# Performance work log

Measured on AMD Instinct MI355X. Metric: run time of the kernel, lower is better.

The kernel has to match this reference:

```python
import jax, jax.numpy as jnp
import numpy as np

H = 8      # n_heads
DK = 64    # d_k per head
EPS = 1e-5       # InstanceNorm1d eps
SLOPE = 0.01     # LeakyReLU negative slope


def setup_inputs() -> dict:
    key = jax.random.key(0)
    ks = jax.random.split(key, 6)
    B, C, L = 16, 256, 1024
    HD = H * DK  # 512
    return {
        "x": jax.random.normal(ks[0], (B, C, L), dtype=jnp.float32),
        "Wq": jax.random.normal(ks[1], (HD, C), dtype=jnp.float32) * 0.02,
        "Wk": jax.random.normal(ks[2], (HD, C), dtype=jnp.float32) * 0.02,
        "Wv": jax.random.normal(ks[3], (HD, C), dtype=jnp.float32) * 0.02,
        "Wo": jax.random.normal(ks[4], (C, HD), dtype=jnp.float32) * 0.02,
        "gamma": jax.random.normal(ks[5], (1,), dtype=jnp.float32),
    }


def reference(x, Wq, Wk, Wv, Wo, gamma):
    B, C, L = x.shape
    # conv1x1 projections (bias=False) == channel matmuls -> [B, H*DK, L]
    # then reshape/permute into heads: [B, H, L, DK]
    def proj(W):
        y = jnp.einsum('oc,bcl->bol', W, x)          # [B, H*DK, L]
        return y.reshape(B, H, DK, L).transpose(0, 1, 3, 2)  # [B, H, L, DK]

    q, k, v = proj(Wq), proj(Wk), proj(Wv)
    # softmax-free linear attention: (Q K^T / d_k) V
    logits = jnp.einsum('bhld,bhmd->bhlm', q, k) / DK  # [B, H, L, L]
    out = jnp.einsum('bhlm,bhmd->bhld', logits, v)     # [B, H, L, DK]
    # merge heads back to channel-first [B, H*DK, L]
    merged = out.transpose(0, 1, 3, 2).reshape(B, H * DK, L)
    # output conv1x1 -> [B, C, L]
    o = jnp.einsum('oc,bcl->bol', Wo, merged)
    # InstanceNorm1d (affine=False): normalize over L per (b, c)
    mu = jnp.mean(o, axis=-1, keepdims=True)
    var = jnp.var(o, axis=-1, keepdims=True)
    o = (o - mu) * jax.lax.rsqrt(var + EPS)
    # gamma-scaled residual + LeakyReLU
    y = o * gamma + x
    return jnp.where(y >= 0, y, SLOPE * y)
```

## Files before the change

### kernel.cpp

```cpp
#include <hip/hip_runtime.h>

typedef __bf16 bf16;
typedef bf16 bf16x8 __attribute__((ext_vector_type(8)));
typedef bf16 bf16x4 __attribute__((ext_vector_type(4)));
typedef float f32x4 __attribute__((ext_vector_type(4)));

#define EPS 1e-5f
#define SLOPE 0.01f

__device__ __forceinline__ void gld_lds16(const bf16* g, bf16* l) {
    __builtin_amdgcn_global_load_lds(
        (const __attribute__((address_space(1))) unsigned int*)g,
        (__attribute__((address_space(3))) unsigned int*)l, 16, 0, 0);
}

__global__ __launch_bounds__(256) void prep_kernel(
    const float* __restrict__ x,
    const float* __restrict__ Wq, const float* __restrict__ Wk,
    const float* __restrict__ Wv, const float* __restrict__ Wo,
    bf16* __restrict__ xT, bf16* __restrict__ xB,
    bf16* __restrict__ WkB, bf16* __restrict__ WvB,
    bf16* __restrict__ WoB, bf16* __restrict__ WqT)
{
    __shared__ float tile[64][65];
    const int id = blockIdx.x;
    const int t = threadIdx.x;
    if (id < 1024) {
        const int lt = id & 15, ct = (id >> 4) & 3, b = id >> 6;
        {
            const int cl = t >> 2;
            const int l4 = (t & 3) << 4;
            const float* src = x + (size_t)(b * 256 + ct * 64 + cl) * 1024 + lt * 64 + l4;
            float4 v0 = ((const float4*)src)[0];
            float4 v1 = ((const float4*)src)[1];
            float4 v2 = ((const float4*)src)[2];
            float4 v3 = ((const float4*)src)[3];
            bf16x8 r0, r1;
            r0[0]=(bf16)v0.x; r0[1]=(bf16)v0.y; r0[2]=(bf16)v0.z; r0[3]=(bf16)v0.w;
            r0[4]=(bf16)v1.x; r0[5]=(bf16)v1.y; r0[6]=(bf16)v1.z; r0[7]=(bf16)v1.w;
            r1[0]=(bf16)v2.x; r1[1]=(bf16)v2.y; r1[2]=(bf16)v2.z; r1[3]=(bf16)v2.w;
            r1[4]=(bf16)v3.x; r1[5]=(bf16)v3.y; r1[6]=(bf16)v3.z; r1[7]=(bf16)v3.w;
            bf16* xbd = xB + (size_t)(b * 256 + ct * 64 + cl) * 1024 + lt * 64 + l4;
            *(bf16x8*)xbd = r0;
            *(bf16x8*)(xbd + 8) = r1;
            float* tr = &tile[cl][l4];
            tr[0]=v0.x; tr[1]=v0.y; tr[2]=v0.z; tr[3]=v0.w;
            tr[4]=v1.x; tr[5]=v1.y; tr[6]=v1.z; tr[7]=v1.w;
            tr[8]=v2.x; tr[9]=v2.y; tr[10]=v2.z; tr[11]=v2.w;
            tr[12]=v3.x; tr[13]=v3.y; tr[14]=v3.z; tr[15]=v3.w;
        }
        __syncthreads();
        {
            const int lw = t >> 2;
            const int ec = (t & 3) << 4;
            bf16x8 o0, o1;
            #pragma unroll
            for (int ii = 0; ii < 8; ++ii) {
                o0[ii] = (bf16)tile[ec + ii][lw];
                o1[ii] = (bf16)tile[ec + 8 + ii][lw];
            }
            bf16* dst = xT + (size_t)(b * 1024 + lt * 64 + lw) * 256 + ct * 64 + ec;
            *(bf16x8*)dst = o0;
            *(bf16x8*)(dst + 8) = o1;
        }
    } else if (id < 1408) {
        const int i = (id - 1024) * 1024 + t * 4;
        const float* src; bf16* dst;
        if (i < 131072)      { src = Wk + i;            dst = WkB + i; }
        else if (i < 262144) { src = Wv + (i - 131072); dst = WvB + (i - 131072); }
        else                 { src = Wo + (i - 262144); dst = WoB + (i - 262144); }
        float4 v = *(const float4*)src;
        bf16x4 o;
        o[0]=(bf16)v.x; o[1]=(bf16)v.y; o[2]=(bf16)v.z; o[3]=(bf16)v.w;
        *(bf16x4*)dst = o;
    } else {
        const int id2 = id - 1408;
        const int h = id2 >> 2, ct = id2 & 3;
        {
            const int e  = t >> 2;
            const int c4 = (t & 3) << 4;
            const float* src = Wq + (size_t)(h * 64 + e) * 256 + ct * 64 + c4;
            float4 v0 = ((const float4*)src)[0];
            float4 v1 = ((const float4*)src)[1];
            float4 v2 = ((const float4*)src)[2];
            float4 v3 = ((const float4*)src)[3];
            float* tr = &tile[e][c4];
            tr[0]=v0.x; tr[1]=v0.y; tr[2]=v0.z; tr[3]=v0.w;
            tr[4]=v1.x; tr[5]=v1.y; tr[6]=v1.z; tr[7]=v1.w;
            tr[8]=v2.x; tr[9]=v2.y; tr[10]=v2.z; tr[11]=v2.w;
            tr[12]=v3.x; tr[13]=v3.y; tr[14]=v3.z; tr[15]=v3.w;
        }
        __syncthreads();
        {
            const int c  = t >> 2;
            const int e4 = (t & 3) << 4;
            bf16x8 o0, o1;
            #pragma unroll
            for (int ii = 0; ii < 8; ++ii) {
                o0[ii] = (bf16)tile[e4 + ii][c];
                o1[ii] = (bf16)tile[e4 + 8 + ii][c];
            }
            bf16* dst = WqT + (size_t)h * 16384 + (size_t)(ct * 64 + c) * 64 + e4;
            *(bf16x8*)dst = o0;
            *(bf16x8*)(dst + 8) = o1;
        }
    }
}

template<int KDIM, typename OutT>
__global__ __launch_bounds__(256) void gemm128_bt(
    const bf16* __restrict__ A, const bf16* __restrict__ Bt, OutT* __restrict__ C,
    long long sA, long long sBt, long long sC, int ldC)
{
    constexpr int NT = KDIM / 32;
    constexpr int NB = 5;
    __shared__ bf16 As[NB][128 * 32];
    __shared__ bf16 Bs[NB][128 * 32];
    const int z = blockIdx.z;
    A  += (size_t)z * sA;
    Bt += (size_t)z * sBt;
    C  += (size_t)z * sC;
    const int m0 = blockIdx.x * 128;
    const int n0 = blockIdx.y * 128;
    const int t = threadIdx.x, w = t >> 6, l = t & 63;
    const int srow = w * 16 + (l >> 2);
    const int ske  = (l & 3) * 8;
    const bf16* ga = A  + (size_t)(m0 + srow) * KDIM + ske;
    const bf16* gb = Bt + (size_t)(n0 + srow) * KDIM + ske;
    const int loff = srow * 32 + ske;
    const int lm = l & 15, lq = l >> 4;
    const int wm = (w & 1) * 64, wn = (w >> 1) * 64;

    #pragma unroll
    for (int i = 0; i < NB - 1; ++i) {
        const int k0 = i * 32;
        gld_lds16(ga + k0, &As[i][0] + loff);
        gld_lds16(ga + k0 + (size_t)64 * KDIM, &As[i][0] + 64 * 32 + loff);
        gld_lds16(gb + k0, &Bs[i][0] + loff);
        gld_lds16(gb + k0 + (size_t)64 * KDIM, &Bs[i][0] + 64 * 32 + loff);
    }

    f32x4 acc[4][4] = {};
    #pragma unroll
    for (int kt = 0; kt < NT; ++kt) {
        const int cur = kt % NB;
        const int stg = (kt + NB - 1) % NB;
        const int remain = NT - 1 - kt;
        if (remain >= 3)      asm volatile("s_waitcnt vmcnt(12)" ::: "memory");
        else if (remain == 2) asm volatile("s_waitcnt vmcnt(8)"  ::: "memory");
        else if (remain == 1) asm volatile("s_waitcnt vmcnt(4)"  ::: "memory");
        else                  asm volatile("s_waitcnt vmcnt(0)"  ::: "memory");
        __builtin_amdgcn_s_barrier();
        __builtin_amdgcn_sched_barrier(0);
        if (kt + NB - 1 < NT) {
            const int k0 = (kt + NB - 1) * 32;
            gld_lds16(ga + k0, &As[stg][0] + loff);
            gld_lds16(ga + k0 + (size_t)64 * KDIM, &As[stg][0] + 64 * 32 + loff);
            gld_lds16(gb + k0, &Bs[stg][0] + loff);
            gld_lds16(gb + k0 + (size_t)64 * KDIM, &Bs[stg][0] + 64 * 32 + loff);
        }
        bf16x8 af[4], bfr[4];
        #pragma unroll
        for (int i = 0; i < 4; ++i)
            af[i] = *(const bf16x8*)(&As[cur][0] + (wm + i * 16 + lm) * 32 + lq * 8);
        #pragma unroll
        for (int j = 0; j < 4; ++j)
            bfr[j] = *(const bf16x8*)(&Bs[cur][0] + (wn + j * 16 + lm) * 32 + lq * 8);
        #pragma unroll
        for (int i = 0; i < 4; ++i)
            #pragma unroll
            for (int j = 0; j < 4; ++j)
                acc[i][j] = __builtin_amdgcn_mfma_f32_16x16x32_bf16(af[i], bfr[j], acc[i][j], 0, 0, 0);
    }
    #pragma unroll
    for (int i = 0; i < 4; ++i)
        #pragma unroll
        for (int j = 0; j < 4; ++j) {
            const int row = m0 + wm + i * 16 + lq * 4;
            const int col = n0 + wn + j * 16 + lm;
            OutT* cp = C + (size_t)row * ldC + col;
            #pragma unroll
            for (int r = 0; r < 4; ++r)
                cp[(size_t)r * ldC] = (OutT)acc[i][j][r];
        }
}

template<int KDIM, typename OutT>
__global__ __launch_bounds__(256) void gemm64_bt(
    const bf16* __restrict__ A, const bf16* __restrict__ Bt, OutT* __restrict__ C,
    long long sA, long long sBt, long long sC, int ldC)
{
    constexpr int NT = KDIM / 32;
    constexpr int NB = 5;
    __shared__ bf16 As[NB][64 * 32];
    __shared__ bf16 Bs[NB][64 * 32];
    const int z = blockIdx.z;
    A  += (size_t)z * sA;
    Bt += (size_t)z * sBt;
    C  += (size_t)z * sC;
    const int m0 = blockIdx.x * 64;
    const int n0 = blockIdx.y * 64;
    const int t = threadIdx.x, w = t >> 6, l = t & 63;
    const int srow = t >> 2;
    const int ske  = (t & 3) * 8;
    const bf16* ga = A  + (size_t)(m0 + srow) * KDIM + ske;
    const bf16* gb = Bt + (size_t)(n0 + srow) * KDIM + ske;
    const int loff = srow * 32 + ske;
    const int lm = l & 15, lq = l >> 4;

    #pragma unroll
    for (int i = 0; i < NB - 1; ++i) {
        const int k0 = i * 32;
        gld_lds16(ga + k0, &As[i][0] + loff);
        gld_lds16(gb + k0, &Bs[i][0] + loff);
    }

    f32x4 acc[4] = {};
    #pragma unroll
    for (int kt = 0; kt < NT; ++kt) {
        const int cur = kt % NB;
        const int stg = (kt + NB - 1) % NB;
        const int remain = NT - 1 - kt;
        if (remain >= 3)      asm volatile("s_waitcnt vmcnt(6)" ::: "memory");
        else if (remain == 2) asm volatile("s_waitcnt vmcnt(4)" ::: "memory");
        else if (remain == 1) asm volatile("s_waitcnt vmcnt(2)" ::: "memory");
        else                  asm volatile("s_waitcnt vmcnt(0)" ::: "memory");
        __builtin_amdgcn_s_barrier();
        __builtin_amdgcn_sched_barrier(0);
        if (kt + NB - 1 < NT) {
            const int k0 = (kt + NB - 1) * 32;
            gld_lds16(ga + k0, &As[stg][0] + loff);
            gld_lds16(gb + k0, &Bs[stg][0] + loff);
        }
        bf16x8 af = *(const bf16x8*)(&As[cur][0] + (w * 16 + lm) * 32 + lq * 8);
        bf16x8 bfr[4];
        #pragma unroll
        for (int j = 0; j < 4; ++j)
            bfr[j] = *(const bf16x8*)(&Bs[cur][0] + (j * 16 + lm) * 32 + lq * 8);
        #pragma unroll
        for (int j = 0; j < 4; ++j)
            acc[j] = __builtin_amdgcn_mfma_f32_16x16x32_bf16(af, bfr[j], acc[j], 0, 0, 0);
    }
    #pragma unroll
    for (int j = 0; j < 4; ++j) {
        const int row = m0 + w * 16 + lq * 4;
        const int col = n0 + j * 16 + lm;
        OutT* cp = C + (size_t)row * ldC + col;
        #pragma unroll
        for (int r = 0; r < 4; ++r)
            cp[(size_t)r * ldC] = (OutT)acc[j][r];
    }
}

__global__ __launch_bounds__(256) void tm_kernel(
    const bf16* __restrict__ S, const bf16* __restrict__ WkB,
    const bf16* __restrict__ WqT, bf16* __restrict__ WmT)
{
    __shared__ __align__(16) bf16 Sc[2][8192];
    __shared__ __align__(16) bf16 Kc[2][8192];
    __shared__ __align__(16) bf16 Qb[16384];
    __shared__ __align__(16) bf16 Tb[4096];

    const int bh = blockIdx.x;
    const int b = bh >> 3, h = bh & 7;
    const bf16* Sg = S   + (size_t)b * 131072 + (size_t)h * 64 * 256;
    const bf16* Kg = WkB + (size_t)h * 64 * 256;
    const bf16* Qg = WqT + (size_t)h * 16384;
    const int t = threadIdx.x, w = t >> 6, l = t & 63;
    const int lm = l & 15, lq = l >> 4;

    #pragma unroll
    for (int it = 0; it < 4; ++it) {
        const int idx = it * 256 + t;
        const int r = idx >> 4, s2 = idx & 15;
        const int gs = (s2 ^ (r & 7)) * 8;
        gld_lds16(Sg + (size_t)r * 256 + gs, &Sc[0][0] + r * 128 + s2 * 8);
        gld_lds16(Kg + (size_t)r * 256 + gs, &Kc[0][0] + r * 128 + s2 * 8);
    }
    #pragma unroll
    for (int it = 0; it < 8; ++it) {
        const int idx = it * 256 + t;
        const int r = idx >> 3, s2 = idx & 7;
        gld_lds16(Qg + (size_t)r * 64 + (s2 ^ (r & 7)) * 8, Qb + r * 64 + s2 * 8);
    }
    #pragma unroll
    for (int it = 0; it < 4; ++it) {
        const int idx = it * 256 + t;
        const int r = idx >> 4, s2 = idx & 15;
        const int gs = (s2 ^ (r & 7)) * 8;
        gld_lds16(Sg + (size_t)r * 256 + 128 + gs, &Sc[1][0] + r * 128 + s2 * 8);
        gld_lds16(Kg + (size_t)r * 256 + 128 + gs, &Kc[1][0] + r * 128 + s2 * 8);
    }

    f32x4 accT[4] = {};
    asm volatile("s_waitcnt vmcnt(16)" ::: "memory");
    __builtin_amdgcn_s_barrier();
    __builtin_amdgcn_sched_barrier(0);
    #pragma unroll
    for (int ks = 0; ks < 4; ++ks) {
        const int q = ks * 4 + lq;
        const int ra = w * 16 + lm;
        bf16x8 a = *(const bf16x8*)(&Sc[0][0] + ra * 128 + (q ^ (ra & 7)) * 8);
        #pragma unroll
        for (int nf = 0; nf < 4; ++nf) {
            const int rb = nf * 16 + lm;
            bf16x8 bb = *(const bf16x8*)(&Kc[0][0] + rb * 128 + (q ^ (rb & 7)) * 8);
            accT[nf] = __builtin_amdgcn_mfma_f32_16x16x32_bf16(a, bb, accT[nf], 0, 0, 0);
        }
    }
    asm volatile("s_waitcnt vmcnt(0)" ::: "memory");
    __builtin_amdgcn_s_barrier();
    __builtin_amdgcn_sched_barrier(0);
    #pragma unroll
    for (int ks = 0; ks < 4; ++ks) {
        const int q = ks * 4 + lq;
        const int ra = w * 16 + lm;
        bf16x8 a = *(const bf16x8*)(&Sc[1][0] + ra * 128 + (q ^ (ra & 7)) * 8);
        #pragma unroll
        for (int nf = 0; nf < 4; ++nf) {
            const int rb = nf * 16 + lm;
            bf16x8 bb = *(const bf16x8*)(&Kc[1][0] + rb * 128 + (q ^ (rb & 7)) * 8);
            accT[nf] = __builtin_amdgcn_mfma_f32_16x16x32_bf16(a, bb, accT[nf], 0, 0, 0);
        }
    }
    #pragma unroll
    for (int nf = 0; nf < 4; ++nf)
        #pragma unroll
        for (int ri = 0; ri < 4; ++ri) {
            const int row = w * 16 + lq * 4 + ri;
            const int col = nf * 16 + lm;
            Tb[row * 64 + (((col >> 3) ^ (row & 7)) << 3) + (col & 7)] =
                (bf16)(accT[nf][ri] * 0.015625f);
        }
    __syncthreads();

    f32x4 accM[4][4] = {};
    #pragma unroll
    for (int ks = 0; ks < 2; ++ks) {
        const int q = ks * 4 + lq;
        bf16x8 bfrag[4];
        #pragma unroll
        for (int nf = 0; nf < 4; ++nf) {
            const int rb = nf * 16 + lm;
            bfrag[nf] = *(const bf16x8*)(Tb + rb * 64 + (q ^ (rb & 7)) * 8);
        }
        #pragma unroll
        for (int mf = 0; mf < 4; ++mf) {
            const int ra = w * 64 + mf * 16 + lm;
            bf16x8 a = *(const bf16x8*)(Qb + ra * 64 + (q ^ (ra & 7)) * 8);
            #pragma unroll
            for (int nf = 0; nf < 4; ++nf)
                accM[mf][nf] = __builtin_amdgcn_mfma_f32_16x16x32_bf16(a, bfrag[nf], accM[mf][nf], 0, 0, 0);
        }
    }
    bf16* Wg = WmT + (size_t)b * 131072 + h * 64;
    #pragma unroll
    for (int mf = 0; mf < 4; ++mf)
        #pragma unroll
        for (int nf = 0; nf < 4; ++nf)
            #pragma unroll
            for (int ri = 0; ri < 4; ++ri) {
                const int c = w * 64 + mf * 16 + lq * 4 + ri;
                const int d = nf * 16 + lm;
                Wg[(size_t)c * 512 + d] = (bf16)accM[mf][nf][ri];
            }
}

__global__ __launch_bounds__(256) void norm_kernel(
    const bf16* __restrict__ o, const bf16* __restrict__ xB,
    const float* __restrict__ gamma, float* __restrict__ y)
{
    const size_t row = blockIdx.x;
    const bf16* orow = o + row * 1024;
    const bf16* xrow = xB + row * 1024;
    float* yrow = y + row * 1024;
    const int tid = threadIdx.x;

    bf16x4 ov = *(const bf16x4*)(orow + tid * 4);
    float4 v = {(float)ov[0], (float)ov[1], (float)ov[2], (float)ov[3]};
    float s  = v.x + v.y + v.z + v.w;
    float ss = v.x * v.x + v.y * v.y + v.z * v.z + v.w * v.w;
    #pragma unroll
    for (int off = 32; off > 0; off >>= 1) {
        s  += __shfl_down(s, off);
        ss += __shfl_down(ss, off);
    }
    __shared__ float red[10];
    const int wave = tid >> 6, lane = tid & 63;
    if (lane == 0) { red[wave] = s; red[4 + wave] = ss; }
    __syncthreads();
    if (tid == 0) {
        float a  = red[0] + red[1] + red[2] + red[3];
        float b2 = red[4] + red[5] + red[6] + red[7];
        float mu = a * (1.0f / 1024.0f);
        float var = b2 * (1.0f / 1024.0f) - mu * mu;
        red[8] = mu;
        red[9] = rsqrtf(var + EPS);
    }
    __syncthreads();
    const float mu = red[8], inv = red[9], g = gamma[0];
    bf16x4 xv4 = *(const bf16x4*)(xrow + tid * 4);
    float4 r;
    r.x = (v.x - mu) * inv * g + (float)xv4[0];
    r.y = (v.y - mu) * inv * g + (float)xv4[1];
    r.z = (v.z - mu) * inv * g + (float)xv4[2];
    r.w = (v.w - mu) * inv * g + (float)xv4[3];
    r.x = r.x >= 0.f ? r.x : SLOPE * r.x;
    r.y = r.y >= 0.f ? r.y : SLOPE * r.y;
    r.z = r.z >= 0.f ? r.z : SLOPE * r.z;
    r.w = r.w >= 0.f ? r.w : SLOPE * r.w;
    ((float4*)yrow)[tid] = r;
}

extern "C" void kernel_launch(void* const* d_in, const int* in_sizes, int n_in,
                              void* d_out, int out_size, void* d_ws, size_t ws_size,
                              hipStream_t stream) {
    const float* x     = (const float*)d_in[0];
    const float* Wq    = (const float*)d_in[1];
    const float* Wk    = (const float*)d_in[2];
    const float* Wv    = (const float*)d_in[3];
    const float* Wo    = (const float*)d_in[4];
    const float* gamma = (const float*)d_in[5];
    float* y = (float*)d_out;

    char* wsb = (char*)d_ws;
    bf16* xT  = (bf16*)(wsb);
    bf16* xB  = (bf16*)(wsb +  8388608);
    bf16* WkB = (bf16*)(wsb + 16777216);
    bf16* WvB = (bf16*)(wsb + 17039360);
    bf16* WoB = (bf16*)(wsb + 17301504);
    bf16* WqT = (bf16*)(wsb + 17563648);
    bf16* G   = (bf16*)(wsb + 17825792);
    bf16* S   = (bf16*)(wsb + 19922944);
    bf16* WmT = (bf16*)(wsb + 24117248);
    bf16* Wt  = (bf16*)(wsb + 28311552);
    bf16* o   = (bf16*)(wsb + 30408704);

    prep_kernel<<<dim3(1440), 256, 0, stream>>>(x, Wq, Wk, Wv, Wo, xT, xB, WkB, WvB, WoB, WqT);

    gemm64_bt<1024, bf16><<<dim3(4, 4, 16), 256, 0, stream>>>(
        xB, xB, G, 262144LL, 262144LL, 65536LL, 256);

    gemm64_bt<256, bf16><<<dim3(8, 4, 16), 256, 0, stream>>>(
        WvB, G, S, 0LL, 65536LL, 131072LL, 256);

    tm_kernel<<<dim3(128), 256, 0, stream>>>(S, WkB, WqT, WmT);

    gemm64_bt<512, bf16><<<dim3(4, 4, 16), 256, 0, stream>>>(
        WoB, WmT, Wt, 0LL, 131072LL, 65536LL, 256);

    gemm128_bt<256, bf16><<<dim3(2, 8, 16), 256, 0, stream>>>(
        Wt, xT, o, 65536LL, 262144LL, 262144LL, 1024);

    norm_kernel<<<dim3(4096), 256, 0, stream>>>(o, xB, gamma, y);
}
```

Baseline: 123.8 us.

## Fuse five GEMM/tm launches into one cooperative persistent kernel with grid syncs

Replaces the five separate launches (Gram GEMM, V projection, per-head tm, Wo GEMM, final output GEMM) with one cooperative kernel of 256 blocks. Stages are separated by grid-wide barriers, and shared memory is held in a union sized for the largest stage. The aim is to remove per-launch overhead and tail gaps between the small dependent kernels. The cost is grid.sync latency, occupancy limited by the largest LDS footprint, and idle blocks during the tm stage, which only uses 128 blocks.

```diff
diff --git a/kernel.cpp b/kernel.cpp
--- a/kernel.cpp
+++ b/kernel.cpp
@@ -1,4 +1,7 @@
 #include <hip/hip_runtime.h>
+#include <hip/hip_cooperative_groups.h>
+
+namespace cg = cooperative_groups;
 
 typedef __bf16 bf16;
 typedef bf16 bf16x8 __attribute__((ext_vector_type(8)));
@@ -107,22 +110,80 @@
     }
 }
 
-template<int KDIM, typename OutT>
-__global__ __launch_bounds__(256) void gemm128_bt(
-    const bf16* __restrict__ A, const bf16* __restrict__ Bt, OutT* __restrict__ C,
-    long long sA, long long sBt, long long sC, int ldC)
+struct __align__(16) SmG64  { bf16 As[5][64 * 32];  bf16 Bs[5][64 * 32];  };
+struct __align__(16) SmG128 { bf16 As[5][128 * 32]; bf16 Bs[5][128 * 32]; };
+struct __align__(16) SmTm   { bf16 Sc[2][8192]; bf16 Kc[2][8192];
+                              bf16 Qb[16384];  bf16 Tb[4096]; };
+union __align__(16) SmAll { SmG64 g64; SmG128 g128; SmTm tm; };
+
+template<int KDIM>
+__device__ __forceinline__ void gemm64_body(SmG64& s,
+    const bf16* __restrict__ A, const bf16* __restrict__ Bt, bf16* __restrict__ C,
+    int m0, int n0, int ldC, int t)
 {
     constexpr int NT = KDIM / 32;
     constexpr int NB = 5;
-    __shared__ bf16 As[NB][128 * 32];
-    __shared__ bf16 Bs[NB][128 * 32];
-    const int z = blockIdx.z;
-    A  += (size_t)z * sA;
-    Bt += (size_t)z * sBt;
-    C  += (size_t)z * sC;
-    const int m0 = blockIdx.x * 128;
-    const int n0 = blockIdx.y * 128;
-    const int t = threadIdx.x, w = t >> 6, l = t & 63;
+    const int w = t >> 6, l = t & 63;
+    const int srow = t >> 2;
+    const int ske  = (t & 3) * 8;
+    const bf16* ga = A  + (size_t)(m0 + srow) * KDIM + ske;
+    const bf16* gb = Bt + (size_t)(n0 + srow) * KDIM + ske;
+    const int loff = srow * 32 + ske;
+    const int lm = l & 15, lq = l >> 4;
+
+    __syncthreads();
+
+    #pragma unroll
+    for (int i = 0; i < NB - 1; ++i) {
+        const int k0 = i * 32;
+        gld_lds16(ga + k0, &s.As[i][0] + loff);
+        gld_lds16(gb + k0, &s.Bs[i][0] + loff);
+    }
+    f32x4 acc[4] = {};
+    #pragma unroll
+    for (int kt = 0; kt < NT; ++kt) {
+        const int cur = kt % NB;
+        const int stg = (kt + NB - 1) % NB;
+        const int remain = NT - 1 - kt;
+        if (remain >= 3)      asm volatile("s_waitcnt vmcnt(6)" ::: "memory");
+        else if (remain == 2) asm volatile("s_waitcnt vmcnt(4)" ::: "memory");
+        else if (remain == 1) asm volatile("s_waitcnt vmcnt(2)" ::: "memory");
+        else                  asm volatile("s_waitcnt vmcnt(0)" ::: "memory");
+        __builtin_amdgcn_s_barrier();
+        __builtin_amdgcn_sched_barrier(0);
+        if (kt + NB - 1 < NT) {
+            const int k0 = (kt + NB - 1) * 32;
+            gld_lds16(ga + k0, &s.As[stg][0] + loff);
+            gld_lds16(gb + k0, &s.Bs[stg][0] + loff);
+        }
+        bf16x8 af = *(const bf16x8*)(&s.As[cur][0] + (w * 16 + lm) * 32 + lq * 8);
+        bf16x8 bfr[4];
+        #pragma unroll
+        for (int j = 0; j < 4; ++j)
+            bfr[j] = *(const bf16x8*)(&s.Bs[cur][0] + (j * 16 + lm) * 32 + lq * 8);
+        #pragma unroll
+        for (int j = 0; j < 4; ++j)
+            acc[j] = __builtin_amdgcn_mfma_f32_16x16x32_bf16(af, bfr[j], acc[j], 0, 0, 0);
+    }
+    #pragma unroll
+    for (int j = 0; j < 4; ++j) {
+        const int row = m0 + w * 16 + lq * 4;
+        const int col = n0 + j * 16 + lm;
+        bf16* cp = C + (size_t)row * ldC + col;
+        #pragma unroll
+        for (int r = 0; r < 4; ++r)
+            cp[(size_t)r * ldC] = (bf16)acc[j][r];
+    }
+}
+
+template<int KDIM>
+__device__ __forceinline__ void gemm128_body(SmG128& s,
+    const bf16* __restrict__ A, const bf16* __restrict__ Bt, bf16* __restrict__ C,
+    int m0, int n0, int ldC, int t)
+{
+    constexpr int NT = KDIM / 32;
+    constexpr int NB = 5;
+    const int w = t >> 6, l = t & 63;
     const int srow = w * 16 + (l >> 2);
     const int ske  = (l & 3) * 8;
     const bf16* ga = A  + (size_t)(m0 + srow) * KDIM + ske;
@@ -131,15 +192,16 @@
     const int lm = l & 15, lq = l >> 4;
     const int wm = (w & 1) * 64, wn = (w >> 1) * 64;
 
+    __syncthreads();
+
     #pragma unroll
     for (int i = 0; i < NB - 1; ++i) {
         const int k0 = i * 32;
-        gld_lds16(ga + k0, &As[i][0] + loff);
-        gld_lds16(ga + k0 + (size_t)64 * KDIM, &As[i][0] + 64 * 32 + loff);
-        gld_lds16(gb + k0, &Bs[i][0] + loff);
-        gld_lds16(gb + k0 + (size_t)64 * KDIM, &Bs[i][0] + 64 * 32 + loff);
-    }
-
+        gld_lds16(ga + k0, &s.As[i][0] + loff);
+        gld_lds16(ga + k0 + (size_t)64 * KDIM, &s.As[i][0] + 64 * 32 + loff);
+        gld_lds16(gb + k0, &s.Bs[i][0] + loff);
+        gld_lds16(gb + k0 + (size_t)64 * KDIM, &s.Bs[i][0] + 64 * 32 + loff);
+    }
     f32x4 acc[4][4] = {};
     #pragma unroll
     for (int kt = 0; kt < NT; ++kt) {
@@ -154,18 +216,18 @@
         __builtin_amdgcn_sched_barrier(0);
         if (kt + NB - 1 < NT) {
             const int k0 = (kt + NB - 1) * 32;
-            gld_lds16(ga + k0, &As[stg][0] + loff);
-            gld_lds16(ga + k0 + (size_t)64 * KDIM, &As[stg][0] + 64 * 32 + loff);
-            gld_lds16(gb + k0, &Bs[stg][0] + loff);
-            gld_lds16(gb + k0 + (size_t)64 * KDIM, &Bs[stg][0] + 64 * 32 + loff);
+            gld_lds16(ga + k0, &s.As[stg][0] + loff);
+            gld_lds16(ga + k0 + (size_t)64 * KDIM, &s.As[stg][0] + 64 * 32 + loff);
+            gld_lds16(gb + k0, &s.Bs[stg][0] + loff);
+            gld_lds16(gb + k0 + (size_t)64 * KDIM, &s.Bs[stg][0] + 64 * 32 + loff);
         }
         bf16x8 af[4], bfr[4];
         #pragma unroll
         for (int i = 0; i < 4; ++i)
-            af[i] = *(const bf16x8*)(&As[cur][0] + (wm + i * 16 + lm) * 32 + lq * 8);
+            af[i] = *(const bf16x8*)(&s.As[cur][0] + (wm + i * 16 + lm) * 32 + lq * 8);
         #pragma unroll
         for (int j = 0; j < 4; ++j)
-            bfr[j] = *(const bf16x8*)(&Bs[cur][0] + (wn + j * 16 + lm) * 32 + lq * 8);
+            bfr[j] = *(const bf16x8*)(&s.Bs[cur][0] + (wn + j * 16 + lm) * 32 + lq * 8);
         #pragma unroll
         for (int i = 0; i < 4; ++i)
             #pragma unroll
@@ -178,95 +240,22 @@
         for (int j = 0; j < 4; ++j) {
             const int row = m0 + wm + i * 16 + lq * 4;
             const int col = n0 + wn + j * 16 + lm;
-            OutT* cp = C + (size_t)row * ldC + col;
+            bf16* cp = C + (size_t)row * ldC + col;
             #pragma unroll
             for (int r = 0; r < 4; ++r)
-                cp[(size_t)r * ldC] = (OutT)acc[i][j][r];
-        }
-}
-
-template<int KDIM, typename OutT>
-__global__ __launch_bounds__(256) void gemm64_bt(
-    const bf16* __restrict__ A, const bf16* __restrict__ Bt, OutT* __restrict__ C,
-    long long sA, long long sBt, long long sC, int ldC)
-{
-    constexpr int NT = KDIM / 32;
-    constexpr int NB = 5;
-    __shared__ bf16 As[NB][64 * 32];
-    __shared__ bf16 Bs[NB][64 * 32];
-    const int z = blockIdx.z;
-    A  += (size_t)z * sA;
-    Bt += (size_t)z * sBt;
-    C  += (size_t)z * sC;
-    const int m0 = blockIdx.x * 64;
-    const int n0 = blockIdx.y * 64;
-    const int t = threadIdx.x, w = t >> 6, l = t & 63;
-    const int srow = t >> 2;
-    const int ske  = (t & 3) * 8;
-    const bf16* ga = A  + (size_t)(m0 + srow) * KDIM + ske;
-    const bf16* gb = Bt + (size_t)(n0 + srow) * KDIM + ske;
-    const int loff = srow * 32 + ske;
-    const int lm = l & 15, lq = l >> 4;
-
-    #pragma unroll
-    for (int i = 0; i < NB - 1; ++i) {
-        const int k0 = i * 32;
-        gld_lds16(ga + k0, &As[i][0] + loff);
-        gld_lds16(gb + k0, &Bs[i][0] + loff);
-    }
-
-    f32x4 acc[4] = {};
-    #pragma unroll
-    for (int kt = 0; kt < NT; ++kt) {
-        const int cur = kt % NB;
-        const int stg = (kt + NB - 1) % NB;
-        const int remain = NT - 1 - kt;
-        if (remain >= 3)      asm volatile("s_waitcnt vmcnt(6)" ::: "memory");
-        else if (remain == 2) asm volatile("s_waitcnt vmcnt(4)" ::: "memory");
-        else if (remain == 1) asm volatile("s_waitcnt vmcnt(2)" ::: "memory");
-        else                  asm volatile("s_waitcnt vmcnt(0)" ::: "memory");
-        __builtin_amdgcn_s_barrier();
-        __builtin_amdgcn_sched_barrier(0);
-        if (kt + NB - 1 < NT) {
-            const int k0 = (kt + NB - 1) * 32;
-            gld_lds16(ga + k0, &As[stg][0] + loff);
-            gld_lds16(gb + k0, &Bs[stg][0] + loff);
-        }
-        bf16x8 af = *(const bf16x8*)(&As[cur][0] + (w * 16 + lm) * 32 + lq * 8);
-        bf16x8 bfr[4];
-        #pragma unroll
-        for (int j = 0; j < 4; ++j)
-            bfr[j] = *(const bf16x8*)(&Bs[cur][0] + (j * 16 + lm) * 32 + lq * 8);
-        #pragma unroll
-        for (int j = 0; j < 4; ++j)
-            acc[j] = __builtin_amdgcn_mfma_f32_16x16x32_bf16(af, bfr[j], acc[j], 0, 0, 0);
-    }
-    #pragma unroll
-    for (int j = 0; j < 4; ++j) {
-        const int row = m0 + w * 16 + lq * 4;
-        const int col = n0 + j * 16 + lm;
-        OutT* cp = C + (size_t)row * ldC + col;
-        #pragma unroll
-        for (int r = 0; r < 4; ++r)
-            cp[(size_t)r * ldC] = (OutT)acc[j][r];
-    }
-}
-
-__global__ __launch_bounds__(256) void tm_kernel(
+                cp[(size_t)r * ldC] = (bf16)acc[i][j][r];
+        }
+}
+
+__device__ __forceinline__ void tm_body(SmTm& sm,
     const bf16* __restrict__ S, const bf16* __restrict__ WkB,
-    const bf16* __restrict__ WqT, bf16* __restrict__ WmT)
-{
-    __shared__ __align__(16) bf16 Sc[2][8192];
-    __shared__ __align__(16) bf16 Kc[2][8192];
-    __shared__ __align__(16) bf16 Qb[16384];
-    __shared__ __align__(16) bf16 Tb[4096];
-
-    const int bh = blockIdx.x;
+    const bf16* __restrict__ WqT, bf16* __restrict__ WmT, int bh, int t)
+{
     const int b = bh >> 3, h = bh & 7;
-    const bf16* Sg = S   + (size_t)b * 131072 + (size_t)h * 64 * 256;
-    const bf16* Kg = WkB + (size_t)h * 64 * 256;
+    const bf16* Sg = S   + (size_t)b * 131072 + (size_t)h * 16384;
+    const bf16* Kg = WkB + (size_t)h * 16384;
     const bf16* Qg = WqT + (size_t)h * 16384;
-    const int t = threadIdx.x, w = t >> 6, l = t & 63;
+    const int w = t >> 6, l = t & 63;
     const int lm = l & 15, lq = l >> 4;
 
     #pragma unroll
@@ -274,22 +263,22 @@
         const int idx = it * 256 + t;
         const int r = idx >> 4, s2 = idx & 15;
         const int gs = (s2 ^ (r & 7)) * 8;
-        gld_lds16(Sg + (size_t)r * 256 + gs, &Sc[0][0] + r * 128 + s2 * 8);
-        gld_lds16(Kg + (size_t)r * 256 + gs, &Kc[0][0] + r * 128 + s2 * 8);
+        gld_lds16(Sg + (size_t)r * 256 + gs, &sm.Sc[0][0] + r * 128 + s2 * 8);
+        gld_lds16(Kg + (size_t)r * 256 + gs, &sm.Kc[0][0] + r * 128 + s2 * 8);
     }
     #pragma unroll
     for (int it = 0; it < 8; ++it) {
         const int idx = it * 256 + t;
         const int r = idx >> 3, s2 = idx & 7;
-        gld_lds16(Qg + (size_t)r * 64 + (s2 ^ (r & 7)) * 8, Qb + r * 64 + s2 * 8);
+        gld_lds16(Qg + (size_t)r * 64 + (s2 ^ (r & 7)) * 8, sm.Qb + r * 64 + s2 * 8);
     }
     #pragma unroll
     for (int it = 0; it < 4; ++it) {
         const int idx = it * 256 + t;
         const int r = idx >> 4, s2 = idx & 15;
         const int gs = (s2 ^ (r & 7)) * 8;
-        gld_lds16(Sg + (size_t)r * 256 + 128 + gs, &Sc[1][0] + r * 128 + s2 * 8);
-        gld_lds16(Kg + (size_t)r * 256 + 128 + gs, &Kc[1][0] + r * 128 + s2 * 8);
+        gld_lds16(Sg + (size_t)r * 256 + 128 + gs, &sm.Sc[1][0] + r * 128 + s2 * 8);
+        gld_lds16(Kg + (size_t)r * 256 + 128 + gs, &sm.Kc[1][0] + r * 128 + s2 * 8);
     }
 
     f32x4 accT[4] = {};
@@ -300,11 +289,11 @@
     for (int ks = 0; ks < 4; ++ks) {
         const int q = ks * 4 + lq;
         const int ra = w * 16 + lm;
-        bf16x8 a = *(const bf16x8*)(&Sc[0][0] + ra * 128 + (q ^ (ra & 7)) * 8);
+        bf16x8 a = *(const bf16x8*)(&sm.Sc[0][0] + ra * 128 + (q ^ (ra & 7)) * 8);
         #pragma unroll
         for (int nf = 0; nf < 4; ++nf) {
             const int rb = nf * 16 + lm;
-            bf16x8 bb = *(const bf16x8*)(&Kc[0][0] + rb * 128 + (q ^ (rb & 7)) * 8);
+            bf16x8 bb = *(const bf16x8*)(&sm.Kc[0][0] + rb * 128 + (q ^ (rb & 7)) * 8);
             accT[nf] = __builtin_amdgcn_mfma_f32_16x16x32_bf16(a, bb, accT[nf], 0, 0, 0);
         }
     }
@@ -315,11 +304,11 @@
     for (int ks = 0; ks < 4; ++ks) {
         const int q = ks * 4 + lq;
         const int ra = w * 16 + lm;
-        bf16x8 a = *(const bf16x8*)(&Sc[1][0] + ra * 128 + (q ^ (ra & 7)) * 8);
+        bf16x8 a = *(const bf16x8*)(&sm.Sc[1][0] + ra * 128 + (q ^ (ra & 7)) * 8);
         #pragma unroll
         for (int nf = 0; nf < 4; ++nf) {
             const int rb = nf * 16 + lm;
-            bf16x8 bb = *(const bf16x8*)(&Kc[1][0] + rb * 128 + (q ^ (rb & 7)) * 8);
+            bf16x8 bb = *(const bf16x8*)(&sm.Kc[1][0] + rb * 128 + (q ^ (rb & 7)) * 8);
             accT[nf] = __builtin_amdgcn_mfma_f32_16x16x32_bf16(a, bb, accT[nf], 0, 0, 0);
         }
     }
@@ -329,7 +318,7 @@
         for (int ri = 0; ri < 4; ++ri) {
             const int row = w * 16 + lq * 4 + ri;
             const int col = nf * 16 + lm;
-            Tb[row * 64 + (((col >> 3) ^ (row & 7)) << 3) + (col & 7)] =
+            sm.Tb[row * 64 + (((col >> 3) ^ (row & 7)) << 3) + (col & 7)] =
                 (bf16)(accT[nf][ri] * 0.015625f);
         }
     __syncthreads();
@@ -342,12 +331,12 @@
         #pragma unroll
         for (int nf = 0; nf < 4; ++nf) {
             const int rb = nf * 16 + lm;
-            bfrag[nf] = *(const bf16x8*)(Tb + rb * 64 + (q ^ (rb & 7)) * 8);
+            bfrag[nf] = *(const bf16x8*)(sm.Tb + rb * 64 + (q ^ (rb & 7)) * 8);
         }
         #pragma unroll
         for (int mf = 0; mf < 4; ++mf) {
             const int ra = w * 64 + mf * 16 + lm;
-            bf16x8 a = *(const bf16x8*)(Qb + ra * 64 + (q ^ (ra & 7)) * 8);
+            bf16x8 a = *(const bf16x8*)(sm.Qb + ra * 64 + (q ^ (ra & 7)) * 8);
             #pragma unroll
             for (int nf = 0; nf < 4; ++nf)
                 accM[mf][nf] = __builtin_amdgcn_mfma_f32_16x16x32_bf16(a, bfrag[nf], accM[mf][nf], 0, 0, 0);
@@ -364,6 +353,50 @@
                 const int d = nf * 16 + lm;
                 Wg[(size_t)c * 512 + d] = (bf16)accM[mf][nf][ri];
             }
+}
+
+__global__ __launch_bounds__(256) void mega_kernel(
+    const bf16* __restrict__ xB, const bf16* __restrict__ xT,
+    const bf16* __restrict__ WkB, const bf16* __restrict__ WvB,
+    const bf16* __restrict__ WoB, const bf16* __restrict__ WqT,
+    bf16* __restrict__ G, bf16* __restrict__ S, bf16* __restrict__ WmT,
+    bf16* __restrict__ Wt, bf16* __restrict__ o)
+{
+    __shared__ SmAll sm;
+    cg::grid_group grid = cg::this_grid();
+    const int t = threadIdx.x;
+    const int bid = blockIdx.x;
+
+    {
+        const int z = bid >> 4, mx = (bid >> 2) & 3, my = bid & 3;
+        gemm64_body<1024>(sm.g64, xB + (size_t)z * 262144, xB + (size_t)z * 262144,
+                          G + (size_t)z * 65536, mx * 64, my * 64, 256, t);
+    }
+    __threadfence(); grid.sync();
+
+    for (int i = 0; i < 2; ++i) {
+        const int tid = i * 256 + bid;
+        const int z = tid >> 5, mx = (tid >> 2) & 7, my = tid & 3;
+        gemm64_body<256>(sm.g64, WvB, G + (size_t)z * 65536,
+                         S + (size_t)z * 131072, mx * 64, my * 64, 256, t);
+    }
+    __threadfence(); grid.sync();
+
+    if (bid < 128) tm_body(sm.tm, S, WkB, WqT, WmT, bid, t);
+    __threadfence(); grid.sync();
+
+    {
+        const int z = bid >> 4, mx = (bid >> 2) & 3, my = bid & 3;
+        gemm64_body<512>(sm.g64, WoB, WmT + (size_t)z * 131072,
+                         Wt + (size_t)z * 65536, mx * 64, my * 64, 256, t);
+    }
+    __threadfence(); grid.sync();
+
+    {
+        const int z = bid >> 4, mx = (bid >> 3) & 1, my = bid & 7;
+        gemm128_body<256>(sm.g128, Wt + (size_t)z * 65536, xT + (size_t)z * 262144,
+                          o + (size_t)z * 262144, mx * 128, my * 128, 1024, t);
+    }
 }
 
 __global__ __launch_bounds__(256) void norm_kernel(
@@ -438,19 +471,14 @@
 
     prep_kernel<<<dim3(1440), 256, 0, stream>>>(x, Wq, Wk, Wv, Wo, xT, xB, WkB, WvB, WoB, WqT);
 
-    gemm64_bt<1024, bf16><<<dim3(4, 4, 16), 256, 0, stream>>>(
-        xB, xB, G, 262144LL, 262144LL, 65536LL, 256);
-
-    gemm64_bt<256, bf16><<<dim3(8, 4, 16), 256, 0, stream>>>(
-        WvB, G, S, 0LL, 65536LL, 131072LL, 256);
-
-    tm_kernel<<<dim3(128), 256, 0, stream>>>(S, WkB, WqT, WmT);
-
-    gemm64_bt<512, bf16><<<dim3(4, 4, 16), 256, 0, stream>>>(
-        WoB, WmT, Wt, 0LL, 131072LL, 65536LL, 256);
-
-    gemm128_bt<256, bf16><<<dim3(2, 8, 16), 256, 0, stream>>>(
-        Wt, xT, o, 65536LL, 262144LL, 262144LL, 1024);
+    const bf16* xBa = xB;  const bf16* xTa = xT;
+    const bf16* WkBa = WkB; const bf16* WvBa = WvB;
+    const bf16* WoBa = WoB; const bf16* WqTa = WqT;
+    bf16* Ga = G; bf16* Sa = S; bf16* WmTa = WmT; bf16* Wta = Wt; bf16* oa = o;
+    void* margs[] = { &xBa, &xTa, &WkBa, &WvBa, &WoBa, &WqTa,
+                      &Ga, &Sa, &WmTa, &Wta, &oa };
+    hipLaunchCooperativeKernel((const void*)mega_kernel, dim3(256), dim3(256),
+                               margs, 0, stream);
 
     norm_kernel<<<dim3(4096), 256, 0, stream>>>(o, xB, gamma, y);
 }
```

New measurement: 359.1 us. 190% more time.

## Fuse Wv·G projection GEMM into the per-head tm kernel

Applied to the files above, without the earlier changes.

Removes the separate GEMM that computed S = Wv·G for all heads and instead computes each head's 64x256 slice of it inside the tm kernel, staging G through a ring of four LDS buffers with async global-to-LDS loads. The intermediate S no longer round-trips through global memory, and one kernel launch goes away. In exchange, each of the 128 blocks now rereads the full per-batch G matrix (eight heads each load the same G), and this phase runs with only 128 blocks, so GPU occupancy for that work is lower than the former 512-block GEMM.

```diff
diff --git a/kernel.cpp b/kernel.cpp
--- a/kernel.cpp
+++ b/kernel.cpp
@@ -252,74 +252,128 @@
     }
 }
 
-__global__ __launch_bounds__(256) void tm_kernel(
-    const bf16* __restrict__ S, const bf16* __restrict__ WkB,
-    const bf16* __restrict__ WqT, bf16* __restrict__ WmT)
+struct __align__(16) Tm2Ph1 { bf16 P[16384]; bf16 Va[16384]; bf16 Gr[4][8192]; };
+struct __align__(16) Tm2Ph2 { bf16 P[16384]; bf16 Kc[16384]; bf16 Qb[16384]; bf16 Tb[4096]; };
+union  __align__(16) Tm2Sm  { Tm2Ph1 p1; Tm2Ph2 p2; };
+
+__global__ __launch_bounds__(256) void tm2_kernel(
+    const bf16* __restrict__ G, const bf16* __restrict__ WvB,
+    const bf16* __restrict__ WkB, const bf16* __restrict__ WqT,
+    bf16* __restrict__ WmT)
 {
-    __shared__ __align__(16) bf16 Sc[2][8192];
-    __shared__ __align__(16) bf16 Kc[2][8192];
-    __shared__ __align__(16) bf16 Qb[16384];
-    __shared__ __align__(16) bf16 Tb[4096];
-
+    __shared__ Tm2Sm sm;
     const int bh = blockIdx.x;
     const int b = bh >> 3, h = bh & 7;
-    const bf16* Sg = S   + (size_t)b * 131072 + (size_t)h * 64 * 256;
-    const bf16* Kg = WkB + (size_t)h * 64 * 256;
+    const bf16* Gg = G   + (size_t)b * 65536;
+    const bf16* Vg = WvB + (size_t)h * 16384;
+    const bf16* Kg = WkB + (size_t)h * 16384;
     const bf16* Qg = WqT + (size_t)h * 16384;
     const int t = threadIdx.x, w = t >> 6, l = t & 63;
     const int lm = l & 15, lq = l >> 4;
 
+    {
+        const int rb = t >> 2 << 2;
+    }
     #pragma unroll
     for (int it = 0; it < 4; ++it) {
         const int idx = it * 256 + t;
-        const int r = idx >> 4, s2 = idx & 15;
-        const int gs = (s2 ^ (r & 7)) * 8;
-        gld_lds16(Sg + (size_t)r * 256 + gs, &Sc[0][0] + r * 128 + s2 * 8);
-        gld_lds16(Kg + (size_t)r * 256 + gs, &Kc[0][0] + r * 128 + s2 * 8);
+        const int r = idx >> 2, s2 = idx & 3;
+        gld_lds16(Gg + (size_t)r * 256 + 0 * 32 + (s2 ^ (r & 3)) * 8,
+                  &sm.p1.Gr[0][0] + r * 32 + s2 * 8);
+    }
+    #pragma unroll
+    for (int it = 0; it < 8; ++it) {
+        const int idx = it * 256 + t;
+        const int r = idx >> 5, s = idx & 31;
+        gld_lds16(Vg + (size_t)r * 256 + (s ^ (r & 7)) * 8,
+                  sm.p1.Va + r * 256 + s * 8);
+    }
+    #pragma unroll
+    for (int tb = 1; tb < 3; ++tb) {
+        #pragma unroll
+        for (int it = 0; it < 4; ++it) {
+            const int idx = it * 256 + t;
+            const int r = idx >> 2, s2 = idx & 3;
+            gld_lds16(Gg + (size_t)r * 256 + tb * 32 + (s2 ^ (r & 3)) * 8,
+                      &sm.p1.Gr[tb][0] + r * 32 + s2 * 8);
+        }
+    }
+
+    f32x4 accP[4][4] = {};
+    #pragma unroll
+    for (int kt = 0; kt < 8; ++kt) {
+        if (kt <= 5)      asm volatile("s_waitcnt vmcnt(8)" ::: "memory");
+        else if (kt == 6) asm volatile("s_waitcnt vmcnt(4)" ::: "memory");
+        else              asm volatile("s_waitcnt vmcnt(0)" ::: "memory");
+        __builtin_amdgcn_s_barrier();
+        __builtin_amdgcn_sched_barrier(0);
+        if (kt < 5) {
+            const int tb = kt + 3;
+            #pragma unroll
+            for (int it = 0; it < 4; ++it) {
+                const int idx = it * 256 + t;
+                const int r = idx >> 2, s2 = idx & 3;
+                gld_lds16(Gg + (size_t)r * 256 + tb * 32 + (s2 ^ (r & 3)) * 8,
+                          &sm.p1.Gr[tb & 3][0] + r * 32 + s2 * 8);
+            }
+        }
+        bf16x8 af[4], bfr[4];
+        #pragma unroll
+        for (int mf = 0; mf < 4; ++mf) {
+            const int ra = mf * 16 + lm;
+            af[mf] = *(const bf16x8*)(sm.p1.Va + ra * 256 + ((kt * 4 + lq) ^ (ra & 7)) * 8);
+        }
+        #pragma unroll
+        for (int nf = 0; nf < 4; ++nf) {
+            const int rb = w * 64 + nf * 16 + lm;
+            bfr[nf] = *(const bf16x8*)(&sm.p1.Gr[kt & 3][0] + rb * 32 + (lq ^ (rb & 3)) * 8);
+        }
+        #pragma unroll
+        for (int mf = 0; mf < 4; ++mf)
+            #pragma unroll
+            for (int nf = 0; nf < 4; ++nf)
+                accP[mf][nf] = __builtin_amdgcn_mfma_f32_16x16x32_bf16(af[mf], bfr[nf], accP[mf][nf], 0, 0, 0);
+    }
+    #pragma unroll
+    for (int mf = 0; mf < 4; ++mf)
+        #pragma unroll
+        for (int nf = 0; nf < 4; ++nf)
+            #pragma unroll
+            for (int ri = 0; ri < 4; ++ri) {
+                const int d = mf * 16 + lq * 4 + ri;
+                const int c = w * 64 + nf * 16 + lm;
+                sm.p1.P[d * 256 + (((c >> 3) ^ (d & 7)) << 3) + (c & 7)] =
+                    (bf16)accP[mf][nf][ri];
+            }
+    __syncthreads();
+
+    #pragma unroll
+    for (int it = 0; it < 8; ++it) {
+        const int idx = it * 256 + t;
+        const int r = idx >> 5, s = idx & 31;
+        gld_lds16(Kg + (size_t)r * 256 + (s ^ (r & 7)) * 8,
+                  sm.p2.Kc + r * 256 + s * 8);
     }
     #pragma unroll
     for (int it = 0; it < 8; ++it) {
         const int idx = it * 256 + t;
         const int r = idx >> 3, s2 = idx & 7;
-        gld_lds16(Qg + (size_t)r * 64 + (s2 ^ (r & 7)) * 8, Qb + r * 64 + s2 * 8);
-    }
-    #pragma unroll
-    for (int it = 0; it < 4; ++it) {
-        const int idx = it * 256 + t;
-        const int r = idx >> 4, s2 = idx & 15;
-        const int gs = (s2 ^ (r & 7)) * 8;
-        gld_lds16(Sg + (size_t)r * 256 + 128 + gs, &Sc[1][0] + r * 128 + s2 * 8);
-        gld_lds16(Kg + (size_t)r * 256 + 128 + gs, &Kc[1][0] + r * 128 + s2 * 8);
-    }
-
-    f32x4 accT[4] = {};
-    asm volatile("s_waitcnt vmcnt(16)" ::: "memory");
+        gld_lds16(Qg + (size_t)r * 64 + (s2 ^ (r & 7)) * 8,
+                  sm.p2.Qb + r * 64 + s2 * 8);
+    }
+
+    asm volatile("s_waitcnt vmcnt(8)" ::: "memory");
     __builtin_amdgcn_s_barrier();
     __builtin_amdgcn_sched_barrier(0);
-    #pragma unroll
-    for (int ks = 0; ks < 4; ++ks) {
-        const int q = ks * 4 + lq;
+    f32x4 accT[4] = {};
+    #pragma unroll
+    for (int kk = 0; kk < 8; ++kk) {
         const int ra = w * 16 + lm;
-        bf16x8 a = *(const bf16x8*)(&Sc[0][0] + ra * 128 + (q ^ (ra & 7)) * 8);
+        bf16x8 a = *(const bf16x8*)(sm.p2.P + ra * 256 + ((kk * 4 + lq) ^ (ra & 7)) * 8);
         #pragma unroll
         for (int nf = 0; nf < 4; ++nf) {
             const int rb = nf * 16 + lm;
-            bf16x8 bb = *(const bf16x8*)(&Kc[0][0] + rb * 128 + (q ^ (rb & 7)) * 8);
-            accT[nf] = __builtin_amdgcn_mfma_f32_16x16x32_bf16(a, bb, accT[nf], 0, 0, 0);
-        }
-    }
-    asm volatile("s_waitcnt vmcnt(0)" ::: "memory");
-    __builtin_amdgcn_s_barrier();
-    __builtin_amdgcn_sched_barrier(0);
-    #pragma unroll
-    for (int ks = 0; ks < 4; ++ks) {
-        const int q = ks * 4 + lq;
-        const int ra = w * 16 + lm;
-        bf16x8 a = *(const bf16x8*)(&Sc[1][0] + ra * 128 + (q ^ (ra & 7)) * 8);
-        #pragma unroll
-        for (int nf = 0; nf < 4; ++nf) {
-            const int rb = nf * 16 + lm;
-            bf16x8 bb = *(const bf16x8*)(&Kc[1][0] + rb * 128 + (q ^ (rb & 7)) * 8);
+            bf16x8 bb = *(const bf16x8*)(sm.p2.Kc + rb * 256 + ((kk * 4 + lq) ^ (rb & 7)) * 8);
             accT[nf] = __builtin_amdgcn_mfma_f32_16x16x32_bf16(a, bb, accT[nf], 0, 0, 0);
         }
     }
@@ -329,9 +383,10 @@
         for (int ri = 0; ri < 4; ++ri) {
             const int row = w * 16 + lq * 4 + ri;
             const int col = nf * 16 + lm;
-            Tb[row * 64 + (((col >> 3) ^ (row & 7)) << 3) + (col & 7)] =
+            sm.p2.Tb[row * 64 + (((col >> 3) ^ (row & 7)) << 3) + (col & 7)] =
                 (bf16)(accT[nf][ri] * 0.015625f);
         }
+    asm volatile("s_waitcnt vmcnt(0)" ::: "memory");
     __syncthreads();
 
     f32x4 accM[4][4] = {};
@@ -342,12 +397,12 @@
         #pragma unroll
         for (int nf = 0; nf < 4; ++nf) {
             const int rb = nf * 16 + lm;
-            bfrag[nf] = *(const bf16x8*)(Tb + rb * 64 + (q ^ (rb & 7)) * 8);
+            bfrag[nf] = *(const bf16x8*)(sm.p2.Tb + rb * 64 + (q ^ (rb & 7)) * 8);
         }
         #pragma unroll
         for (int mf = 0; mf < 4; ++mf) {
             const int ra = w * 64 + mf * 16 + lm;
-            bf16x8 a = *(const bf16x8*)(Qb + ra * 64 + (q ^ (ra & 7)) * 8);
+            bf16x8 a = *(const bf16x8*)(sm.p2.Qb + ra * 64 + (q ^ (ra & 7)) * 8);
             #pragma unroll
             for (int nf = 0; nf < 4; ++nf)
                 accM[mf][nf] = __builtin_amdgcn_mfma_f32_16x16x32_bf16(a, bfrag[nf], accM[mf][nf], 0, 0, 0);
@@ -431,7 +486,6 @@
     bf16* WoB = (bf16*)(wsb + 17301504);
     bf16* WqT = (bf16*)(wsb + 17563648);
     bf16* G   = (bf16*)(wsb + 17825792);
-    bf16* S   = (bf16*)(wsb + 19922944);
     bf16* WmT = (bf16*)(wsb + 24117248);
     bf16* Wt  = (bf16*)(wsb + 28311552);
     bf16* o   = (bf16*)(wsb + 30408704);
@@ -441,10 +495,7 @@
     gemm64_bt<1024, bf16><<<dim3(4, 4, 16), 256, 0, stream>>>(
         xB, xB, G, 262144LL, 262144LL, 65536LL, 256);
 
-    gemm64_bt<256, bf16><<<dim3(8, 4, 16), 256, 0, stream>>>(
-        WvB, G, S, 0LL, 65536LL, 131072LL, 256);
-
-    tm_kernel<<<dim3(128), 256, 0, stream>>>(S, WkB, WqT, WmT);
+    tm2_kernel<<<dim3(128), 256, 0, stream>>>(G, WvB, WkB, WqT, WmT);
 
     gemm64_bt<512, bf16><<<dim3(4, 4, 16), 256, 0, stream>>>(
         WoB, WmT, Wt, 0LL, 131072LL, 65536LL, 256);
```

New measurement: 122.7 us. Within noise of the previous version (-0.9%).
